# Kernel optimization log

Hardware: AMD Instinct MI355X
Metric: run time of the kernel (lower is better)

Reference implementation:

```python
import jax, jax.numpy as jnp
import numpy as np

# --- static config (from init_kwargs) ---
B = 256        # num graphs
NPG = 128      # nodes per graph
EPG = 512      # edges per graph
DIN = 128      # dim_node
D = 256        # dim_hidden
RATIO = 0.5    # causal_ratio
N_RES = int(RATIO * EPG)
BN_EPS = 1e-5


def setup_inputs() -> dict:
    key = jax.random.key(0)
    ks = jax.random.split(key, 24)
    N = B * NPG
    x = jax.random.normal(ks[0], (N, DIN), jnp.float32)
    # edges confined within each graph, contiguous per graph (graph-sorted)
    src = jax.random.randint(ks[1], (B, EPG), 0, NPG)
    dst = jax.random.randint(ks[2], (B, EPG), 0, NPG)
    off = (jnp.arange(B, dtype=jnp.int32) * NPG)[:, None]
    edge_index = jnp.stack([(src + off).reshape(-1), (dst + off).reshape(-1)], 0).astype(jnp.int32)
    batch = jnp.repeat(jnp.arange(B, dtype=jnp.int32), NPG)

    s = 0.05
    def rn(k, shape):
        return jax.random.normal(k, shape, jnp.float32) * s
    p = dict(
        x=x, edge_index=edge_index, batch=batch,
        vemb=rn(ks[3], (1, D)),
        # conv1 GIN mlp: Linear(DIN,2D) -> BN -> ReLU -> Linear(2D,D)
        W1a=rn(ks[4], (DIN, 2 * D)), b1a=jnp.zeros((2 * D,)),
        g1a=jnp.ones((2 * D,)), be1a=jnp.zeros((2 * D,)),
        W1b=rn(ks[5], (2 * D, D)), b1b=jnp.zeros((D,)),
        g1=jnp.ones((D,)), be1=jnp.zeros((D,)),          # outer batch_norm1
        # conv2 GIN mlp
        W2a=rn(ks[6], (D, 2 * D)), b2a=jnp.zeros((2 * D,)),
        g2a=jnp.ones((2 * D,)), be2a=jnp.zeros((2 * D,)),
        W2b=rn(ks[7], (2 * D, D)), b2b=jnp.zeros((D,)),
        g2=jnp.ones((D,)), be2=jnp.zeros((D,)),          # outer batch_norm2
        # edge scorer: Linear(2D, 1)
        Wl=rn(ks[8], (2 * D, 1)), bl=jnp.zeros((1,)),
    )
    return p


def _bn(h, g, b):
    mu = h.mean(0)
    var = jnp.mean((h - mu) ** 2, 0)
    return (h - mu) * jax.lax.rsqrt(var + BN_EPS) * g + b


def reference(x, edge_index, batch, vemb,
              W1a, b1a, g1a, be1a, W1b, b1b, g1, be1,
              W2a, b2a, g2a, be2a, W2b, b2b, g2, be2,
              Wl, bl):
    N = x.shape[0]
    row, col = edge_index[0], edge_index[1]

    def gin(h, Wa, ba, ga, bta, Wb, bb):
        # GINConv, eps=0: mlp(h + sum_{j->i} h_j), aggregate src feats at dst
        agg = jax.ops.segment_sum(h[row], col, num_segments=N)
        z = (h + agg) @ Wa + ba
        z = jax.nn.relu(_bn(z, ga, bta))
        return z @ Wb + bb

    # layer 1: conv1 -> bn -> relu (dropout_rate = 0)
    post = jax.nn.relu(_bn(gin(x, W1a, b1a, g1a, be1a, W1b, b1b), g1, be1))
    # virtual node gather (embedding of index 0, one per graph)
    vfeat = jnp.broadcast_to(vemb[0], (B, D))
    post = post + vfeat[batch]
    # layer 2 (last): conv2 -> bn, no relu
    xn = _bn(gin(post, W2a, b2a, g2a, be2a, W2b, b2b), g2, be2)

    # edge scoring
    erep = jnp.concatenate([xn[row], xn[col]], axis=-1)          # [E, 2D]
    pred = (erep @ Wl + bl.astype(erep.dtype)).reshape(-1)       # [E]

    # per-graph top-k split (equal EPG edges per graph)
    pw = pred.reshape(B, EPG)
    order = jnp.argsort(-pw, axis=1)
    idx_r, idx_d = order[:, :N_RES], order[:, N_RES:]
    causal_w = jnp.take_along_axis(pw, idx_r, 1).reshape(-1)
    conf_w = -jnp.take_along_axis(pw, idx_d, 1).reshape(-1)
    ei = edge_index.reshape(2, B, EPG)
    causal_ei = jnp.take_along_axis(ei, jnp.broadcast_to(idx_r[None], (2, B, N_RES)), axis=2).reshape(2, -1)
    conf_ei = jnp.take_along_axis(ei, jnp.broadcast_to(idx_d[None], (2, B, EPG - N_RES)), axis=2).reshape(2, -1)
    return (causal_ei, causal_w, conf_ei, conf_w, pred)
```

## Files before the change

### kernel.cpp

```cpp
#include <hip/hip_runtime.h>

#define BGR   256
#define NPG   128
#define EPG   512
#define DIN   128
#define DD    256
#define DD2   512
#define NTOT  (BGR * NPG)
#define ETOT  (BGR * EPG)
#define NRES  (EPG / 2)
#define NCHUNK 256
#define MP    136

#define OFF_CEI  0
#define OFF_CW   (2 * BGR * NRES)
#define OFF_FEI  (OFF_CW + BGR * NRES)
#define OFF_FW   (OFF_FEI + 2 * BGR * NRES)
#define OFF_PRED (OFF_FW + BGR * NRES)

typedef unsigned short ushortt;
typedef __attribute__((ext_vector_type(4))) unsigned short us4;
typedef __attribute__((ext_vector_type(8))) unsigned short us8;
typedef __attribute__((ext_vector_type(8))) short short8;
typedef __attribute__((ext_vector_type(4))) float f32x4;

__device__ __forceinline__ ushortt f2bf(float f) {
    unsigned int u = __float_as_uint(f);
    unsigned int r = (u + 0x7fffu + ((u >> 16) & 1u)) >> 16;
    return (ushortt)r;
}
__device__ __forceinline__ float bf2f(ushortt u) {
    return __uint_as_float(((unsigned int)u) << 16);
}

__device__ __forceinline__ void g2lds16(const void* g, void* l) {
    __builtin_amdgcn_global_load_lds(
        (const __attribute__((address_space(1))) unsigned int*)g,
        (__attribute__((address_space(3))) unsigned int*)l, 16, 0, 0);
}

__global__ __launch_bounds__(256) void prep(const float* __restrict__ W1a,
                                            const float* __restrict__ W1b,
                                            const float* __restrict__ W2a,
                                            const float* __restrict__ W2b,
                                            const float* __restrict__ x,
                                            const int* __restrict__ ei,
                                            ushortt* __restrict__ Wt1a,
                                            ushortt* __restrict__ Wt1b,
                                            ushortt* __restrict__ Wt2a,
                                            ushortt* __restrict__ Wt2b,
                                            ushortt* __restrict__ Madj,
                                            ushortt* __restrict__ s1) {
    __shared__ __align__(16) char smem[102400];
    const int t = threadIdx.x;
    if (blockIdx.x < 1792) {
        const int idx = blockIdx.x * 256 + t;
        if (idx < 65536) {
            const int k = idx >> 9, n = idx & 511;
            Wt1a[n * DIN + k] = f2bf(W1a[idx]);
        } else if (idx < 196608) {
            const int i = idx - 65536;
            const int k = i >> 8, n = i & 255;
            Wt1b[n * DD2 + k] = f2bf(W1b[i]);
        } else if (idx < 327680) {
            const int i = idx - 196608;
            const int k = i >> 9, n = i & 511;
            Wt2a[n * DD + k] = f2bf(W2a[i]);
        } else if (idx < 458752) {
            const int i = idx - 327680;
            const int k = i >> 8, n = i & 255;
            Wt2b[n * DD2 + k] = f2bf(W2b[i]);
        }
        return;
    }
    const int b = blockIdx.x - 1792;
    ushortt* Ms = (ushortt*)smem;
    int* cnt = (int*)(smem + 34816);
    ushortt* XT = (ushortt*)(smem + 34816);
    ushortt* Cs = (ushortt*)(smem + 69632);
    const int wave = t >> 6, lane = t & 63;
    const int qd = lane >> 4, r = lane & 15;
    const int wm = (wave >> 1) * 64, wn = (wave & 1) * 64;

    for (int i = t; i < NPG * NPG; i += 256) cnt[i] = 0;
    __syncthreads();
    for (int e = t; e < EPG; e += 256) {
        const int src = ei[b * EPG + e] - b * NPG;
        const int dst = ei[ETOT + b * EPG + e] - b * NPG;
        atomicAdd(&cnt[dst * NPG + src], 1);
    }
    __syncthreads();
#pragma unroll
    for (int k = 0; k < 8; ++k) {
        const int ch = t + k * 256;
        const int m = ch >> 4, sc = (ch & 15) * 8;
        us8 o;
#pragma unroll
        for (int e = 0; e < 8; ++e)
            o[e] = f2bf((float)(cnt[m * NPG + sc + e] + (m == sc + e ? 1 : 0)));
        *(us8*)&Ms[m * MP + sc] = o;
        *(us8*)&Madj[(size_t)b * NPG * NPG + m * NPG + sc] = o;
    }
    __syncthreads();

#pragma unroll
    for (int k = 0; k < 8; ++k) {
        const int ch = t + k * 256;
        const int c = ch & 127, s8 = ch >> 7;
        us8 o;
#pragma unroll
        for (int j = 0; j < 8; ++j)
            o[j] = f2bf(x[(size_t)(b * NPG + s8 * 8 + j) * DIN + c]);
        *(us8*)&XT[c * MP + s8 * 8] = o;
    }
    __syncthreads();

    f32x4 acc[4][4] = {};
#pragma unroll
    for (int ks = 0; ks < 4; ++ks) {
        const int k0 = ks * 32 + qd * 8;
        short8 af[4], bfr[4];
#pragma unroll
        for (int i = 0; i < 4; ++i)
            af[i] = *(const short8*)&Ms[(wm + i * 16 + r) * MP + k0];
#pragma unroll
        for (int j = 0; j < 4; ++j)
            bfr[j] = *(const short8*)&XT[(wn + j * 16 + r) * MP + k0];
#pragma unroll
        for (int i = 0; i < 4; ++i)
#pragma unroll
            for (int j = 0; j < 4; ++j)
                acc[i][j] = __builtin_amdgcn_mfma_f32_16x16x32_bf16(af[i], bfr[j], acc[i][j], 0, 0, 0);
    }
#pragma unroll
    for (int j = 0; j < 4; ++j) {
        const int coll = wn + j * 16 + r;
#pragma unroll
        for (int i = 0; i < 4; ++i)
#pragma unroll
            for (int tt = 0; tt < 4; ++tt)
                Cs[(wm + i * 16 + qd * 4 + tt) * 128 + coll] = f2bf(acc[i][j][tt]);
    }
    __syncthreads();
#pragma unroll
    for (int k = 0; k < 8; ++k) {
        const int ch = t + k * 256;
        const int row = ch >> 4, colc = (ch & 15) * 8;
        *(us8*)&s1[(size_t)(b * NPG + row) * DIN + colc] = *(const us8*)&Cs[row * 128 + colc];
    }
}

#define BM 128
#define BN 128
#define BK 32
__global__ __launch_bounds__(256) void gemm_mfma(const ushortt* __restrict__ A,
                                                 const ushortt* __restrict__ Wt,
                                                 const float* __restrict__ bias,
                                                 ushortt* __restrict__ C,
                                                 float* __restrict__ psum,
                                                 float* __restrict__ psumsq,
                                                 int M, int N, int K) {
    __shared__ __align__(16) ushortt AsB[2][4][BM * BK];
    __shared__ float redS[2][BN];
    __shared__ float redQ[2][BN];
    const int tid  = threadIdx.x;
    const int wave = tid >> 6;
    const int lane = tid & 63;
    const int qd = lane >> 4;
    const int r  = lane & 15;
    const int wm = (wave >> 1) * 64;
    const int wn = (wave & 1) * 64;
    const int m0 = blockIdx.y * BM;
    const int n0 = blockIdx.x * BN;

    f32x4 acc[4][4] = {};

    for (int kb = 0; kb < K; kb += 128) {
        if (kb) __syncthreads();
#pragma unroll
        for (int c4 = 0; c4 < 4; ++c4) {
            const int k0 = kb + c4 * 32;
#pragma unroll
            for (int s = 0; s < 2; ++s) {
                const int o   = wave * 128 + s * 64 + lane;
                const int row = o >> 2;
                const int cg  = o & 3;
                g2lds16(A  + (size_t)(m0 + row) * K + k0 + cg * 8,
                        &AsB[0][c4][(size_t)(wave * 128 + s * 64) * 8]);
                g2lds16(Wt + (size_t)(n0 + row) * K + k0 + cg * 8,
                        &AsB[1][c4][(size_t)(wave * 128 + s * 64) * 8]);
            }
        }
        __syncthreads();
#pragma unroll
        for (int c4 = 0; c4 < 4; ++c4) {
            short8 af[4], bfr[4];
#pragma unroll
            for (int i = 0; i < 4; ++i)
                af[i] = *(const short8*)&AsB[0][c4][(wm + i * 16 + r) * BK + qd * 8];
#pragma unroll
            for (int j = 0; j < 4; ++j)
                bfr[j] = *(const short8*)&AsB[1][c4][(wn + j * 16 + r) * BK + qd * 8];
#pragma unroll
            for (int i = 0; i < 4; ++i)
#pragma unroll
                for (int j = 0; j < 4; ++j)
                    acc[i][j] = __builtin_amdgcn_mfma_f32_16x16x32_bf16(af[i], bfr[j], acc[i][j], 0, 0, 0);
        }
    }
    __syncthreads();

    ushortt* Cs = &AsB[0][0][0];
#pragma unroll
    for (int j = 0; j < 4; ++j) {
        const int coll = wn + j * 16 + r;
        const float bv = bias[n0 + coll];
        float s = 0.0f, q = 0.0f;
#pragma unroll
        for (int i = 0; i < 4; ++i)
#pragma unroll
            for (int t = 0; t < 4; ++t) {
                const float v = acc[i][j][t] + bv;
                Cs[(wm + i * 16 + qd * 4 + t) * BN + coll] = f2bf(v);
                s += v;
                q = fmaf(v, v, q);
            }
        s += __shfl_xor(s, 16); s += __shfl_xor(s, 32);
        q += __shfl_xor(q, 16); q += __shfl_xor(q, 32);
        if (qd == 0) {
            redS[wave >> 1][coll] = s;
            redQ[wave >> 1][coll] = q;
        }
    }
    __syncthreads();
    if (tid < BN) {
        psum[(size_t)blockIdx.y * N + n0 + tid]   = redS[0][tid] + redS[1][tid];
        psumsq[(size_t)blockIdx.y * N + n0 + tid] = redQ[0][tid] + redQ[1][tid];
    }
#pragma unroll
    for (int s8 = 0; s8 < 8; ++s8) {
        const int c    = tid + 256 * s8;
        const int row  = c >> 4;
        const int colc = (c & 15) * 8;
        const us8 v = *(const us8*)&Cs[row * BN + colc];
        *(us8*)&C[(size_t)(m0 + row) * N + n0 + colc] = v;
    }
}

__global__ __launch_bounds__(256) void bn_finalize(const float* __restrict__ psum,
                                                   const float* __restrict__ psumsq,
                                                   const float* __restrict__ g,
                                                   const float* __restrict__ be,
                                                   int ncols,
                                                   float* __restrict__ scale,
                                                   float* __restrict__ shift) {
    const int c = blockIdx.x * 256 + threadIdx.x;
    double s = 0.0, s2 = 0.0;
    for (int k = 0; k < NCHUNK; ++k) {
        s += (double)psum[(size_t)k * ncols + c];
        s2 += (double)psumsq[(size_t)k * ncols + c];
    }
    const double mean = s / (double)NTOT;
    const double var = s2 / (double)NTOT - mean * mean;
    const double rs = 1.0 / sqrt(var + 1e-5);
    const float sc = (float)((double)g[c] * rs);
    scale[c] = sc;
    shift[c] = (float)((double)be[c] - mean * (double)sc);
}

__global__ __launch_bounds__(256) void gemm_bn(const ushortt* __restrict__ A,
                                               const ushortt* __restrict__ Wt,
                                               const float* __restrict__ scale,
                                               const float* __restrict__ shift,
                                               const float* __restrict__ bias,
                                               ushortt* __restrict__ C,
                                               float* __restrict__ psOut,
                                               float* __restrict__ pqOut) {
    __shared__ __align__(16) ushortt AsB[2][4][BM * BK];
    __shared__ float redS[2][BN];
    __shared__ float redQ[2][BN];
    __shared__ float scs[DD2], shs[DD2];
    const int tid  = threadIdx.x;
    const int wave = tid >> 6;
    const int lane = tid & 63;
    const int qd = lane >> 4;
    const int r  = lane & 15;
    const int wm = (wave >> 1) * 64;
    const int wn = (wave & 1) * 64;
    const int m0 = blockIdx.y * BM;
    const int n0 = blockIdx.x * BN;
    const int K = DD2, N = DD;

    for (int i = tid; i < K; i += 256) {
        scs[i] = scale[i];
        shs[i] = shift[i];
    }
    __syncthreads();

    f32x4 acc[4][4] = {};

    for (int kb = 0; kb < K; kb += 128) {
        if (kb) __syncthreads();
#pragma unroll
        for (int c4 = 0; c4 < 4; ++c4) {
            const int k0 = kb + c4 * 32;
#pragma unroll
            for (int s = 0; s < 2; ++s) {
                const int o   = wave * 128 + s * 64 + lane;
                const int row = o >> 2;
                const int cg  = o & 3;
                g2lds16(Wt + (size_t)(n0 + row) * K + k0 + cg * 8,
                        &AsB[1][c4][(size_t)(wave * 128 + s * 64) * 8]);
            }
        }
#pragma unroll
        for (int c4 = 0; c4 < 4; ++c4) {
            const int k0 = kb + c4 * 32;
#pragma unroll
            for (int s = 0; s < 2; ++s) {
                const int o   = wave * 128 + s * 64 + lane;
                const int row = o >> 2;
                const int cg  = o & 3;
                const us8 a8 = *(const us8*)&A[(size_t)(m0 + row) * K + k0 + cg * 8];
                const float4 s4a = *(const float4*)&scs[k0 + cg * 8];
                const float4 s4b = *(const float4*)&scs[k0 + cg * 8 + 4];
                const float4 h4a = *(const float4*)&shs[k0 + cg * 8];
                const float4 h4b = *(const float4*)&shs[k0 + cg * 8 + 4];
                us8 t8;
                t8[0] = f2bf(fmaxf(fmaf(bf2f(a8[0]), s4a.x, h4a.x), 0.0f));
                t8[1] = f2bf(fmaxf(fmaf(bf2f(a8[1]), s4a.y, h4a.y), 0.0f));
                t8[2] = f2bf(fmaxf(fmaf(bf2f(a8[2]), s4a.z, h4a.z), 0.0f));
                t8[3] = f2bf(fmaxf(fmaf(bf2f(a8[3]), s4a.w, h4a.w), 0.0f));
                t8[4] = f2bf(fmaxf(fmaf(bf2f(a8[4]), s4b.x, h4b.x), 0.0f));
                t8[5] = f2bf(fmaxf(fmaf(bf2f(a8[5]), s4b.y, h4b.y), 0.0f));
                t8[6] = f2bf(fmaxf(fmaf(bf2f(a8[6]), s4b.z, h4b.z), 0.0f));
                t8[7] = f2bf(fmaxf(fmaf(bf2f(a8[7]), s4b.w, h4b.w), 0.0f));
                *(us8*)&AsB[0][c4][row * BK + cg * 8] = t8;
            }
        }
        __syncthreads();
#pragma unroll
        for (int c4 = 0; c4 < 4; ++c4) {
            short8 af[4], bfr[4];
#pragma unroll
            for (int i = 0; i < 4; ++i)
                af[i] = *(const short8*)&AsB[0][c4][(wm + i * 16 + r) * BK + qd * 8];
#pragma unroll
            for (int j = 0; j < 4; ++j)
                bfr[j] = *(const short8*)&AsB[1][c4][(wn + j * 16 + r) * BK + qd * 8];
#pragma unroll
            for (int i = 0; i < 4; ++i)
#pragma unroll
                for (int j = 0; j < 4; ++j)
                    acc[i][j] = __builtin_amdgcn_mfma_f32_16x16x32_bf16(af[i], bfr[j], acc[i][j], 0, 0, 0);
        }
    }
    __syncthreads();

    ushortt* Cs = &AsB[0][0][0];
#pragma unroll
    for (int j = 0; j < 4; ++j) {
        const int coll = wn + j * 16 + r;
        const float bv = bias[n0 + coll];
        float s = 0.0f, q = 0.0f;
#pragma unroll
        for (int i = 0; i < 4; ++i)
#pragma unroll
            for (int t = 0; t < 4; ++t) {
                const float v = acc[i][j][t] + bv;
                Cs[(wm + i * 16 + qd * 4 + t) * BN + coll] = f2bf(v);
                s += v;
                q = fmaf(v, v, q);
            }
        s += __shfl_xor(s, 16); s += __shfl_xor(s, 32);
        q += __shfl_xor(q, 16); q += __shfl_xor(q, 32);
        if (qd == 0) {
            redS[wave >> 1][coll] = s;
            redQ[wave >> 1][coll] = q;
        }
    }
    __syncthreads();
    if (tid < BN) {
        psOut[(size_t)blockIdx.y * N + n0 + tid] = redS[0][tid] + redS[1][tid];
        pqOut[(size_t)blockIdx.y * N + n0 + tid] = redQ[0][tid] + redQ[1][tid];
    }
#pragma unroll
    for (int s8 = 0; s8 < 8; ++s8) {
        const int c    = tid + 256 * s8;
        const int row  = c >> 4;
        const int colc = (c & 15) * 8;
        const us8 v = *(const us8*)&Cs[row * BN + colc];
        *(us8*)&C[(size_t)(m0 + row) * N + n0 + colc] = v;
    }
}

__global__ __launch_bounds__(256) void agg2_mm(const ushortt* __restrict__ h,
                                               const float* __restrict__ psum,
                                               const float* __restrict__ psumsq,
                                               const float* __restrict__ g,
                                               const float* __restrict__ be,
                                               const float* __restrict__ vemb,
                                               const ushortt* __restrict__ Madj,
                                               ushortt* __restrict__ s2) {
    __shared__ ushortt Ms[NPG * MP];
    __shared__ ushortt PT[NPG * MP];
    __shared__ double redS[2][128];
    __shared__ double redQ[2][128];
    __shared__ float scs[128], shs[128];
    const int nb = blockIdx.x, b = blockIdx.y, t = threadIdx.x;
    const int wave = t >> 6, lane = t & 63;
    const int qd = lane >> 4, r = lane & 15;
    const int wm = (wave >> 1) * 64, wn = (wave & 1) * 64;
    const ushortt* Mg = Madj + (size_t)b * NPG * NPG;
#pragma unroll
    for (int k = 0; k < 8; ++k) {
        const int ch = t + k * 256;
        const int m = ch >> 4, sc = (ch & 15) * 8;
        *(us8*)&Ms[m * MP + sc] = *(const us8*)&Mg[m * NPG + sc];
    }
    {
        const int cl = t & 127, half = t >> 7;
        const int c = nb * 128 + cl;
        double s = 0.0, q = 0.0;
#pragma unroll 4
        for (int k = half * 128; k < half * 128 + 128; ++k) {
            s += (double)psum[(size_t)k * DD + c];
            q += (double)psumsq[(size_t)k * DD + c];
        }
        redS[half][cl] = s;
        redQ[half][cl] = q;
    }
    __syncthreads();
    if (t < 128) {
        const int c = nb * 128 + t;
        const double s = redS[0][t] + redS[1][t];
        const double q = redQ[0][t] + redQ[1][t];
        const double mean = s / (double)NTOT;
        const double var = q / (double)NTOT - mean * mean;
        const double rs = 1.0 / sqrt(var + 1e-5);
        const float sc = (float)((double)g[c] * rs);
        scs[t] = sc;
        shs[t] = (float)((double)be[c] - mean * (double)sc);
    }
    __syncthreads();
#pragma unroll
    for (int k = 0; k < 8; ++k) {
        const int ch = t + k * 256;
        const int cl = ch & 127, s8 = ch >> 7;
        const float scv = scs[cl], shv = shs[cl], vev = vemb[nb * 128 + cl];
        us8 o;
#pragma unroll
        for (int j = 0; j < 8; ++j) {
            float v = fmaf(bf2f(h[(size_t)(b * NPG + s8 * 8 + j) * DD + nb * 128 + cl]), scv, shv);
            o[j] = f2bf(fmaxf(v, 0.0f) + vev);
        }
        *(us8*)&PT[cl * MP + s8 * 8] = o;
    }
    __syncthreads();
    f32x4 acc[4][4] = {};
#pragma unroll
    for (int ks = 0; ks < 4; ++ks) {
        const int k0 = ks * 32 + qd * 8;
        short8 af[4], bfr[4];
#pragma unroll
        for (int i = 0; i < 4; ++i)
            af[i] = *(const short8*)&Ms[(wm + i * 16 + r) * MP + k0];
#pragma unroll
        for (int j = 0; j < 4; ++j)
            bfr[j] = *(const short8*)&PT[(wn + j * 16 + r) * MP + k0];
#pragma unroll
        for (int i = 0; i < 4; ++i)
#pragma unroll
            for (int j = 0; j < 4; ++j)
                acc[i][j] = __builtin_amdgcn_mfma_f32_16x16x32_bf16(af[i], bfr[j], acc[i][j], 0, 0, 0);
    }
    __syncthreads();
    ushortt* Cs = Ms;
#pragma unroll
    for (int j = 0; j < 4; ++j) {
        const int coll = wn + j * 16 + r;
#pragma unroll
        for (int i = 0; i < 4; ++i)
#pragma unroll
            for (int tt = 0; tt < 4; ++tt)
                Cs[(wm + i * 16 + qd * 4 + tt) * 128 + coll] = f2bf(acc[i][j][tt]);
    }
    __syncthreads();
#pragma unroll
    for (int k = 0; k < 8; ++k) {
        const int ch = t + k * 256;
        const int row = ch >> 4, colc = (ch & 15) * 8;
        *(us8*)&s2[(size_t)(b * NPG + row) * DD + nb * 128 + colc] =
            *(const us8*)&Cs[row * 128 + colc];
    }
}

__global__ __launch_bounds__(EPG) void sort_mega(const ushortt* __restrict__ h2,
                                                 const float* __restrict__ psum,
                                                 const float* __restrict__ psumsq,
                                                 const float* __restrict__ g,
                                                 const float* __restrict__ be,
                                                 const float* __restrict__ Wl,
                                                 const float* __restrict__ bl,
                                                 const int* __restrict__ ei,
                                                 float* __restrict__ out) {
    __shared__ double redS[2][DD];
    __shared__ double redQ[2][DD];
    __shared__ float scs[DD], shs[DD];
    __shared__ float pa[NPG], pb[NPG];
    __shared__ float pw[EPG];
    __shared__ int ord[EPG];
    const int b = blockIdx.x, t = threadIdx.x;
    {
        const int c = t & 255, half = t >> 8;
        double s = 0.0, q = 0.0;
#pragma unroll 4
        for (int k = half * 128; k < half * 128 + 128; ++k) {
            s += (double)psum[(size_t)k * DD + c];
            q += (double)psumsq[(size_t)k * DD + c];
        }
        redS[half][c] = s;
        redQ[half][c] = q;
    }
    __syncthreads();
    if (t < DD) {
        const double s = redS[0][t] + redS[1][t];
        const double q = redQ[0][t] + redQ[1][t];
        const double mean = s / (double)NTOT;
        const double var = q / (double)NTOT - mean * mean;
        const double rs = 1.0 / sqrt(var + 1e-5);
        const float sc = (float)((double)g[t] * rs);
        scs[t] = sc;
        shs[t] = (float)((double)be[t] - mean * (double)sc);
    }
    __syncthreads();
    {
        const int wave = t >> 6, lane = t & 63;
        const float4 w0 = *(const float4*)&Wl[lane * 4];
        const float4 w1 = *(const float4*)&Wl[DD + lane * 4];
        const float4 sc4 = *(const float4*)&scs[lane * 4];
        const float4 sh4 = *(const float4*)&shs[lane * 4];
        for (int n = wave; n < NPG; n += 8) {
            const us4 z4 = *(const us4*)&h2[(size_t)(b * NPG + n) * DD + lane * 4];
            const float x0 = fmaf(bf2f(z4.x), sc4.x, sh4.x);
            const float x1 = fmaf(bf2f(z4.y), sc4.y, sh4.y);
            const float x2 = fmaf(bf2f(z4.z), sc4.z, sh4.z);
            const float x3 = fmaf(bf2f(z4.w), sc4.w, sh4.w);
            float sa = x0 * w0.x + x1 * w0.y + x2 * w0.z + x3 * w0.w;
            float sb = x0 * w1.x + x1 * w1.y + x2 * w1.z + x3 * w1.w;
#pragma unroll
            for (int off = 32; off >= 1; off >>= 1) {
                sa += __shfl_down(sa, off);
                sb += __shfl_down(sb, off);
            }
            if (lane == 0) { pa[n] = sa; pb[n] = sb; }
        }
    }
    __syncthreads();
    const int rl = ei[b * EPG + t] - b * NPG;
    const int cl = ei[ETOT + b * EPG + t] - b * NPG;
    const float v = pa[rl] + pb[cl] + bl[0];
    pw[t] = v;
    out[OFF_PRED + b * EPG + t] = v;
    __syncthreads();
    int rank = 0;
#pragma unroll 8
    for (int k = 0; k < EPG; ++k) {
        const float u = pw[k];
        rank += (u > v) || (u == v && k < t);
    }
    ord[rank] = t;
    __syncthreads();
    const int j = ord[t];
    const float wv = pw[j];
    const float e0 = (float)ei[b * EPG + j];
    const float e1 = (float)ei[ETOT + b * EPG + j];
    if (t < NRES) {
        out[OFF_CEI + b * NRES + t] = e0;
        out[OFF_CEI + BGR * NRES + b * NRES + t] = e1;
        out[OFF_CW + b * NRES + t] = wv;
    } else {
        const int p = t - NRES;
        out[OFF_FEI + b * NRES + p] = e0;
        out[OFF_FEI + BGR * NRES + b * NRES + p] = e1;
        out[OFF_FW + b * NRES + p] = -wv;
    }
}

extern "C" void kernel_launch(void* const* d_in, const int* in_sizes, int n_in,
                              void* d_out, int out_size, void* d_ws, size_t ws_size,
                              hipStream_t stream) {
    (void)in_sizes; (void)n_in; (void)out_size; (void)ws_size;
    const float* x    = (const float*)d_in[0];
    const int*   ei   = (const int*)d_in[1];
    const float* vemb = (const float*)d_in[3];
    const float* W1a  = (const float*)d_in[4];
    const float* b1a  = (const float*)d_in[5];
    const float* g1a  = (const float*)d_in[6];
    const float* be1a = (const float*)d_in[7];
    const float* W1b  = (const float*)d_in[8];
    const float* b1b  = (const float*)d_in[9];
    const float* g1   = (const float*)d_in[10];
    const float* be1  = (const float*)d_in[11];
    const float* W2a  = (const float*)d_in[12];
    const float* b2a  = (const float*)d_in[13];
    const float* g2a  = (const float*)d_in[14];
    const float* be2a = (const float*)d_in[15];
    const float* W2b  = (const float*)d_in[16];
    const float* b2b  = (const float*)d_in[17];
    const float* g2   = (const float*)d_in[18];
    const float* be2  = (const float*)d_in[19];
    const float* Wl   = (const float*)d_in[20];
    const float* bl   = (const float*)d_in[21];
    float* out = (float*)d_out;

    char* wp = (char*)d_ws;
    auto alloc = [&](size_t bytes) -> char* {
        char* r = wp;
        wp += (bytes + 255) & ~(size_t)255;
        return r;
    };
    ushortt* zb    = (ushortt*)alloc((size_t)NTOT * 512 * 2);
    ushortt* bufC  = (ushortt*)alloc((size_t)NTOT * 256 * 2);
    ushortt* bufS1 = (ushortt*)alloc((size_t)NTOT * 128 * 2);
    ushortt* bufS2 = (ushortt*)alloc((size_t)NTOT * 256 * 2);
    ushortt* Madj  = (ushortt*)alloc((size_t)BGR * NPG * NPG * 2);
    ushortt* Wt1a  = (ushortt*)alloc((size_t)DIN * DD2 * 2);
    ushortt* Wt1b  = (ushortt*)alloc((size_t)DD2 * DD * 2);
    ushortt* Wt2a  = (ushortt*)alloc((size_t)DD * DD2 * 2);
    ushortt* Wt2b  = (ushortt*)alloc((size_t)DD2 * DD * 2);
    float*   psA   = (float*)alloc((size_t)256 * DD2 * 4);
    float*   pqA   = (float*)alloc((size_t)256 * DD2 * 4);
    float*   psB   = (float*)alloc((size_t)256 * DD * 4);
    float*   pqB   = (float*)alloc((size_t)256 * DD * 4);
    float*   scA   = (float*)alloc(DD2 * 4);
    float*   shA   = (float*)alloc(DD2 * 4);

    prep<<<2048, 256, 0, stream>>>(W1a, W1b, W2a, W2b, x, ei,
                                   Wt1a, Wt1b, Wt2a, Wt2b, Madj, bufS1);

    gemm_mfma<<<dim3(DD2 / BN, NTOT / BM), 256, 0, stream>>>(bufS1, Wt1a, b1a, zb, psA, pqA, NTOT, DD2, DIN);
    bn_finalize<<<2, 256, 0, stream>>>(psA, pqA, g1a, be1a, DD2, scA, shA);

    gemm_bn<<<dim3(DD / BN, NTOT / BM), 256, 0, stream>>>(zb, Wt1b, scA, shA, b1b, bufC, psB, pqB);

    agg2_mm<<<dim3(2, BGR), 256, 0, stream>>>(bufC, psB, pqB, g1, be1, vemb, Madj, bufS2);

    gemm_mfma<<<dim3(DD2 / BN, NTOT / BM), 256, 0, stream>>>(bufS2, Wt2a, b2a, zb, psA, pqA, NTOT, DD2, DD);
    bn_finalize<<<2, 256, 0, stream>>>(psA, pqA, g2a, be2a, DD2, scA, shA);

    gemm_bn<<<dim3(DD / BN, NTOT / BM), 256, 0, stream>>>(zb, Wt2b, scA, shA, b2b, bufC, psB, pqB);

    sort_mega<<<BGR, EPG, 0, stream>>>(bufC, psB, pqB, g2, be2, Wl, bl, ei, out);
}
```

Before: 302.2 us.

## Rebuild adjacency in LDS from edges instead of storing dense matrix globally

Stops writing the dense per-graph bf16 adjacency matrix (8 MB) to global memory in prep and re-reading it in agg2_mm. Both kernels now build the counts in shared memory from the edge list, using packed 16-bit atomic counters so the count array takes half the LDS. Prep's shared footprint shrinks by aliasing the output tile onto the counter region, which needs an extra barrier and may allow more blocks per CU. In exchange the edge scatter and atomics run twice, once per kernel.

```diff
diff --git a/kernel.cpp b/kernel.cpp
--- a/kernel.cpp
+++ b/kernel.cpp
@@ -49,9 +49,8 @@
                                             ushortt* __restrict__ Wt1b,
                                             ushortt* __restrict__ Wt2a,
                                             ushortt* __restrict__ Wt2b,
-                                            ushortt* __restrict__ Madj,
                                             ushortt* __restrict__ s1) {
-    __shared__ __align__(16) char smem[102400];
+    __shared__ __align__(16) char smem[69632];
     const int t = threadIdx.x;
     if (blockIdx.x < 1792) {
         const int idx = blockIdx.x * 256 + t;
@@ -77,17 +76,18 @@
     ushortt* Ms = (ushortt*)smem;
     int* cnt = (int*)(smem + 34816);
     ushortt* XT = (ushortt*)(smem + 34816);
-    ushortt* Cs = (ushortt*)(smem + 69632);
+    ushortt* Cs = (ushortt*)(smem + 34816);
     const int wave = t >> 6, lane = t & 63;
     const int qd = lane >> 4, r = lane & 15;
     const int wm = (wave >> 1) * 64, wn = (wave & 1) * 64;
 
-    for (int i = t; i < NPG * NPG; i += 256) cnt[i] = 0;
+    for (int i = t; i < NPG * NPG / 2; i += 256) cnt[i] = 0;
     __syncthreads();
     for (int e = t; e < EPG; e += 256) {
         const int src = ei[b * EPG + e] - b * NPG;
         const int dst = ei[ETOT + b * EPG + e] - b * NPG;
-        atomicAdd(&cnt[dst * NPG + src], 1);
+        const int idx = dst * NPG + src;
+        atomicAdd(&cnt[idx >> 1], 1 << ((idx & 1) * 16));
     }
     __syncthreads();
 #pragma unroll
@@ -96,10 +96,12 @@
         const int m = ch >> 4, sc = (ch & 15) * 8;
         us8 o;
 #pragma unroll
-        for (int e = 0; e < 8; ++e)
-            o[e] = f2bf((float)(cnt[m * NPG + sc + e] + (m == sc + e ? 1 : 0)));
+        for (int e = 0; e < 8; ++e) {
+            const int i = m * NPG + sc + e;
+            const int v = ((cnt[i >> 1] >> ((i & 1) * 16)) & 0xffff) + (m == sc + e ? 1 : 0);
+            o[e] = f2bf((float)v);
+        }
         *(us8*)&Ms[m * MP + sc] = o;
-        *(us8*)&Madj[(size_t)b * NPG * NPG + m * NPG + sc] = o;
     }
     __syncthreads();
 
@@ -132,6 +134,7 @@
             for (int j = 0; j < 4; ++j)
                 acc[i][j] = __builtin_amdgcn_mfma_f32_16x16x32_bf16(af[i], bfr[j], acc[i][j], 0, 0, 0);
     }
+    __syncthreads();
 #pragma unroll
     for (int j = 0; j < 4; ++j) {
         const int coll = wn + j * 16 + r;
@@ -400,23 +403,26 @@
                                                const float* __restrict__ g,
                                                const float* __restrict__ be,
                                                const float* __restrict__ vemb,
-                                               const ushortt* __restrict__ Madj,
+                                               const int* __restrict__ ei,
                                                ushortt* __restrict__ s2) {
-    __shared__ ushortt Ms[NPG * MP];
-    __shared__ ushortt PT[NPG * MP];
+    __shared__ __align__(16) ushortt Ms[NPG * MP];
+    __shared__ __align__(16) ushortt PT[NPG * MP];
     __shared__ double redS[2][128];
     __shared__ double redQ[2][128];
     __shared__ float scs[128], shs[128];
+    int* cnt = (int*)PT;
     const int nb = blockIdx.x, b = blockIdx.y, t = threadIdx.x;
     const int wave = t >> 6, lane = t & 63;
     const int qd = lane >> 4, r = lane & 15;
     const int wm = (wave >> 1) * 64, wn = (wave & 1) * 64;
-    const ushortt* Mg = Madj + (size_t)b * NPG * NPG;
-#pragma unroll
-    for (int k = 0; k < 8; ++k) {
-        const int ch = t + k * 256;
-        const int m = ch >> 4, sc = (ch & 15) * 8;
-        *(us8*)&Ms[m * MP + sc] = *(const us8*)&Mg[m * NPG + sc];
+
+    for (int i = t; i < NPG * NPG / 2; i += 256) cnt[i] = 0;
+    __syncthreads();
+    for (int e = t; e < EPG; e += 256) {
+        const int src = ei[b * EPG + e] - b * NPG;
+        const int dst = ei[ETOT + b * EPG + e] - b * NPG;
+        const int idx = dst * NPG + src;
+        atomicAdd(&cnt[idx >> 1], 1 << ((idx & 1) * 16));
     }
     {
         const int cl = t & 127, half = t >> 7;
@@ -431,6 +437,19 @@
         redQ[half][cl] = q;
     }
     __syncthreads();
+#pragma unroll
+    for (int k = 0; k < 8; ++k) {
+        const int ch = t + k * 256;
+        const int m = ch >> 4, sc = (ch & 15) * 8;
+        us8 o;
+#pragma unroll
+        for (int e = 0; e < 8; ++e) {
+            const int i = m * NPG + sc + e;
+            const int v = ((cnt[i >> 1] >> ((i & 1) * 16)) & 0xffff) + (m == sc + e ? 1 : 0);
+            o[e] = f2bf((float)v);
+        }
+        *(us8*)&Ms[m * MP + sc] = o;
+    }
     if (t < 128) {
         const int c = nb * 128 + t;
         const double s = redS[0][t] + redS[1][t];
@@ -624,7 +643,6 @@
     ushortt* bufC  = (ushortt*)alloc((size_t)NTOT * 256 * 2);
     ushortt* bufS1 = (ushortt*)alloc((size_t)NTOT * 128 * 2);
     ushortt* bufS2 = (ushortt*)alloc((size_t)NTOT * 256 * 2);
-    ushortt* Madj  = (ushortt*)alloc((size_t)BGR * NPG * NPG * 2);
     ushortt* Wt1a  = (ushortt*)alloc((size_t)DIN * DD2 * 2);
     ushortt* Wt1b  = (ushortt*)alloc((size_t)DD2 * DD * 2);
     ushortt* Wt2a  = (ushortt*)alloc((size_t)DD * DD2 * 2);
@@ -637,14 +655,14 @@
     float*   shA   = (float*)alloc(DD2 * 4);
 
     prep<<<2048, 256, 0, stream>>>(W1a, W1b, W2a, W2b, x, ei,
-                                   Wt1a, Wt1b, Wt2a, Wt2b, Madj, bufS1);
+                                   Wt1a, Wt1b, Wt2a, Wt2b, bufS1);
 
     gemm_mfma<<<dim3(DD2 / BN, NTOT / BM), 256, 0, stream>>>(bufS1, Wt1a, b1a, zb, psA, pqA, NTOT, DD2, DIN);
     bn_finalize<<<2, 256, 0, stream>>>(psA, pqA, g1a, be1a, DD2, scA, shA);
 
     gemm_bn<<<dim3(DD / BN, NTOT / BM), 256, 0, stream>>>(zb, Wt1b, scA, shA, b1b, bufC, psB, pqB);
 
-    agg2_mm<<<dim3(2, BGR), 256, 0, stream>>>(bufC, psB, pqB, g1, be1, vemb, Madj, bufS2);
+    agg2_mm<<<dim3(2, BGR), 256, 0, stream>>>(bufC, psB, pqB, g1, be1, vemb, ei, bufS2);
 
     gemm_mfma<<<dim3(DD2 / BN, NTOT / BM), 256, 0, stream>>>(bufS2, Wt2a, b2a, zb, psA, pqA, NTOT, DD2, DD);
     bn_finalize<<<2, 256, 0, stream>>>(psA, pqA, g2a, be2a, DD2, scA, shA);
```

Result: no change. 300.6 us (-0.5%).
